# Kernel optimization log

Measured on AMD Instinct MI355X. Metric: run time of the kernel, lower is better.

Reference implementation:

```python
import jax, jax.numpy as jnp
import numpy as np

K, D, N = 32, 128, 65536
EPS = 1e-6


def setup_inputs() -> dict:
    key = jax.random.key(0)
    k1, k2, k3 = jax.random.split(key, 3)
    x = jax.random.normal(k1, (N, D), dtype=jnp.float32)
    means = jax.random.normal(k2, (K, D), dtype=jnp.float32)
    # SPD covariances (original init is identity; use SPD perturbation so Cholesky is valid)
    B = jax.random.normal(k3, (K, D, D), dtype=jnp.float32) * 0.1
    covariances = jnp.einsum('kij,klj->kil', B, B) / D + jnp.eye(D, dtype=jnp.float32)
    weights = jnp.ones((K,), dtype=jnp.float32) / K
    return {"x": x, "means": means, "covariances": covariances, "weights": weights}


def reference(x, means, covariances, weights):
    d = x.shape[-1]
    cov = covariances + EPS * jnp.eye(d, dtype=x.dtype)          # [K,D,D]
    L = jnp.linalg.cholesky(cov)                                 # [K,D,D]
    diff = x[None, :, :] - means[:, None, :]                     # [K,N,D]
    # Mahalanobis via triangular solve: m = ||L^{-1}(x-mu)||^2
    sol = jax.scipy.linalg.solve_triangular(
        L, jnp.swapaxes(diff, 1, 2), lower=True)                 # [K,D,N]
    maha = jnp.sum(sol * sol, axis=1)                            # [K,N]
    half_logdet = jnp.sum(jnp.log(jnp.diagonal(L, axis1=1, axis2=2)), axis=1)  # [K]
    log_prob = (-0.5 * (d * jnp.log(2.0 * jnp.pi) + maha)
                - half_logdet[:, None])                          # [K,N]
    weighted = log_prob.T + jnp.log(weights)                     # [N,K]
    return jax.nn.logsumexp(weighted, axis=1)                    # [N]
```

## Files before the change

### kernel.cpp

```cpp
#include <hip/hip_runtime.h>
#include <hip/hip_bf16.h>
#include <math.h>

#define KCOMP 32
#define DDIM  128
#define NPTS  65536
#define GMM_EPS 1e-6f
#define SA 129
#define UFT 1280

typedef __attribute__((ext_vector_type(8)))  __bf16 bf16x8;
typedef __attribute__((ext_vector_type(16))) float  f32x16;

__device__ __forceinline__ unsigned short f2bf(float f){
  unsigned u = __builtin_bit_cast(unsigned, f);
  u = (u + 0x7FFFu + ((u >> 16) & 1u)) >> 16;
  return (unsigned short)u;
}
__device__ __forceinline__ float rlane(float v, int lsrc){
  return __builtin_bit_cast(float, __builtin_amdgcn_readlane(__builtin_bit_cast(int, v), lsrc));
}

__device__ __noinline__ float chol_inv32(float* __restrict__ Ab,
                                         float* __restrict__ Wb,
                                         const int c){
  float ar[32], lr[32], rd[32], v[32];
  #pragma unroll
  for(int i=0;i<32;i++) ar[i] = Ab[i*SA + c];
  float hl = 0.f;
  #pragma unroll
  for(int j=0;j<32;j++){
    float d   = rlane(ar[j], j);
    float rsd = rsqrtf(d);
    hl += logf(d);
    rd[j] = rsd;
    float Lcj  = ar[j]*rsd;
    lr[j] = (c>=j) ? Lcj : 0.f;
    float coef = Lcj*rsd;
    #pragma unroll
    for(int i=j;i<32;i++){
      float bij = rlane(ar[i], j);
      ar[i] = fmaf(-bij, coef, ar[i]);
    }
  }
  #pragma unroll
  for(int j=0;j<32;j++) Ab[c*SA + j] = lr[j];
  #pragma unroll
  for(int i=0;i<32;i++){
    float s = (i==c) ? 1.f : 0.f;
    #pragma unroll
    for(int p=0;p<i;p++) s = fmaf(-rlane(lr[p], i), v[p], s);
    v[i] = s * rd[i];
  }
  #pragma unroll
  for(int i=0;i<32;i++) Wb[i*SA + c] = v[i];
  return 0.5f*hl;
}

__global__ __launch_bounds__(256) void k_prep(const float* __restrict__ cov,
                                              const float* __restrict__ wts,
                                              const float* __restrict__ means,
                                              float* __restrict__ ws_c3,
                                              unsigned short* __restrict__ qfrag,
                                              unsigned short* __restrict__ ufrag){
  __shared__ float A[DDIM*SA];
  __shared__ float W[DDIM*SA];
  __shared__ float Tb[3*32*33];
  __shared__ float muS[DDIM];
  const int t=threadIdx.x, w=t>>6, l=t&63, k=blockIdx.x;
  const int r0=(l>>3)*4, c0=(l&7)*4;

  const float4* cv4 = (const float4*)(cov + (size_t)k*DDIM*DDIM);
  #pragma unroll
  for(int v=0; v<16; v++){
    int idx4 = t + 256*v; float4 f = cv4[idx4];
    int e = idx4*4; int i = e>>7; int j = e&127;
    float* d = &A[i*SA+j]; d[0]=f.x; d[1]=f.y; d[2]=f.z; d[3]=f.w;
  }
  for(int z=t; z<DDIM*SA; z+=256) W[z] = 0.f;
  if(t<DDIM) muS[t] = means[k*DDIM+t];
  __syncthreads();
  if(t<DDIM) A[t*SA+t] += GMM_EPS;
  __syncthreads();

  static const int SYI[10]={1,2,2,3,3,3, 2,3,3, 3};
  static const int SYJ[10]={1,1,2,1,2,3, 2,2,3, 3};
  static const int SYO[5] ={0,6,9,10,10};

  float hsum = 0.f;
  #pragma unroll 1
  for(int b=0;b<4;b++){
    const int b32=b*32;
    if(w==0) hsum += chol_inv32(&A[b32*SA+b32], &W[b32*SA+b32], l&31);
    __syncthreads();
    if(w < 3-b){
      const int ibl = b+1+w;
      float acc[4][4]={};
      for(int kc=0;kc<32;kc+=4){
        float a_[4][4], b_[4][4];
        #pragma unroll
        for(int e=0;e<4;e++)
          #pragma unroll
          for(int g=0;g<4;g++){
            a_[e][g]=A[(32*ibl+r0+e)*SA + b32+kc+g];
            b_[e][g]=W[(b32+c0+e)*SA   + b32+kc+g];
          }
        #pragma unroll
        for(int e=0;e<4;e++)
          #pragma unroll
          for(int f=0;f<4;f++)
            acc[e][f]+=a_[e][0]*b_[f][0]+a_[e][1]*b_[f][1]
                      +a_[e][2]*b_[f][2]+a_[e][3]*b_[f][3];
      }
      #pragma unroll
      for(int e=0;e<4;e++)
        #pragma unroll
        for(int f=0;f<4;f++)
          A[(32*ibl+r0+e)*SA + b32+c0+f] = acc[e][f];
    }
    __syncthreads();
    #pragma unroll 1
    for(int u=SYO[b]+w; u<SYO[b+1]; u+=4){
      const int ui=SYI[u], uj=SYJ[u];
      float acc[4][4]={};
      for(int kc=0;kc<32;kc+=4){
        float a_[4][4], b_[4][4];
        #pragma unroll
        for(int e=0;e<4;e++)
          #pragma unroll
          for(int g=0;g<4;g++){
            a_[e][g]=A[(32*ui+r0+e)*SA + b32+kc+g];
            b_[e][g]=A[(32*uj+c0+e)*SA + b32+kc+g];
          }
        #pragma unroll
        for(int e=0;e<4;e++)
          #pragma unroll
          for(int f=0;f<4;f++)
            acc[e][f]+=a_[e][0]*b_[f][0]+a_[e][1]*b_[f][1]
                      +a_[e][2]*b_[f][2]+a_[e][3]*b_[f][3];
      }
      #pragma unroll
      for(int e=0;e<4;e++)
        #pragma unroll
        for(int f=0;f<4;f++)
          A[(32*ui+r0+e)*SA+32*uj+c0+f] -= acc[e][f];
    }
    __syncthreads();
  }

  #pragma unroll 1
  for(int lev=1;lev<=3;lev++){
    if(w<4-lev){
      const int j=w, i=w+lev;
      float* T=&Tb[w*1056];
      float acc[4][4]={};
      #pragma unroll 1
      for(int p=j;p<i;p++){
        for(int kc=0;kc<32;kc+=4){
          float a_[4][4], b_[4][4];
          #pragma unroll
          for(int e=0;e<4;e++)
            #pragma unroll
            for(int g=0;g<4;g++){
              a_[e][g]=A[(32*i+r0+e)*SA + 32*p+kc+g];
              b_[e][g]=W[(32*p+kc+e)*SA + 32*j+c0+g];
            }
          #pragma unroll
          for(int e=0;e<4;e++)
            #pragma unroll
            for(int f=0;f<4;f++)
              acc[e][f]+=a_[e][0]*b_[0][f]+a_[e][1]*b_[1][f]
                        +a_[e][2]*b_[2][f]+a_[e][3]*b_[3][f];
        }
      }
      #pragma unroll
      for(int e=0;e<4;e++)
        #pragma unroll
        for(int f=0;f<4;f++)
          T[(r0+e)*33+c0+f]=acc[e][f];
      float ac2[4][4]={};
      for(int kc=0;kc<32;kc+=4){
        float a_[4][4], b_[4][4];
        #pragma unroll
        for(int e=0;e<4;e++)
          #pragma unroll
          for(int g=0;g<4;g++){
            a_[e][g]=W[(32*i+r0+e)*SA + 32*i+kc+g];
            b_[e][g]=T[(kc+e)*33 + c0+g];
          }
        #pragma unroll
        for(int e=0;e<4;e++)
          #pragma unroll
          for(int f=0;f<4;f++)
            ac2[e][f]+=a_[e][0]*b_[0][f]+a_[e][1]*b_[1][f]
                      +a_[e][2]*b_[2][f]+a_[e][3]*b_[3][f];
      }
      #pragma unroll
      for(int e=0;e<4;e++)
        #pragma unroll
        for(int f=0;f<4;f++)
          W[(32*i+r0+e)*SA+32*j+c0+f] = -ac2[e][f];
    }
    __syncthreads();
  }

  if(t<DDIM){
    float s=0.f;
    #pragma unroll 8
    for(int c=0;c<DDIM;c++) s += W[t*SA+c]*muS[c];
    Tb[t]=s;
  }
  __syncthreads();
  if(t<DDIM){
    float s=0.f;
    #pragma unroll 8
    for(int r=0;r<DDIM;r++) s += W[r*SA+t]*Tb[r];
    Tb[128+t]=s;
  }
  __syncthreads();
  if(w==0){
    float p = Tb[l]*Tb[l] + Tb[l+64]*Tb[l+64];
    #pragma unroll
    for(int off=32; off; off>>=1) p += __shfl_xor(p, off);
    if(l==0) ws_c3[k] = logf(wts[k]) - hsum - 117.6241322f - 0.5f*p;
  }
  if(t<16){
    int tile=t>>1, half=t&1;
    const float* qq=&Tb[128 + tile*16 + half*8];
    unsigned uu[4];
    #pragma unroll
    for(int h2=0;h2<4;h2++){
      unsigned lo=f2bf(qq[2*h2]), hi=f2bf(qq[2*h2+1]);
      uu[h2]=lo|(hi<<16);
    }
    uint4 wv; wv.x=uu[0]; wv.y=uu[1]; wv.z=uu[2]; wv.w=uu[3];
    ((uint4*)qfrag)[tile*64 + half*32 + k] = wv;
  }
  #pragma unroll 1
  for(int s0=t;s0<UFT;s0+=256){
    int tile=s0>>6, l2=s0&63;
    int db = (tile<2)?0:((tile<6)?1:((tile<12)?2:3));
    int kc = tile - ((db==0)?0:((db==1)?2:((db==2)?6:12)));
    int row=db*32+(l2&31), colb=kc*16+((l2>>5)<<3);
    unsigned uu[4];
    #pragma unroll
    for(int h2=0;h2<4;h2++){
      unsigned lo=f2bf(W[row*SA+colb+2*h2]);
      unsigned hi=f2bf(W[row*SA+colb+2*h2+1]);
      uu[h2]=lo|(hi<<16);
    }
    uint4 wv; wv.x=uu[0]; wv.y=uu[1]; wv.z=uu[2]; wv.w=uu[3];
    ((uint4*)ufrag)[(size_t)k*UFT+s0]=wv;
  }
}

#define MFMA_B(acc,u,xv) acc=__builtin_amdgcn_mfma_f32_32x32x16_bf16(__builtin_bit_cast(bf16x8,u),xv,acc,0,0,0)

__global__ __launch_bounds__(512,2) void k_main(const float* __restrict__ x,
                                                const uint4* __restrict__ uf,
                                                const uint4* __restrict__ qf,
                                                const float* __restrict__ ws_c3,
                                                float* __restrict__ out){
  __shared__ uint4 xs[4*8*64];
  __shared__ float lin[KCOMP*128];
  __shared__ float mahaS[4*8*128];
  __shared__ float c3s[KCOMP];
  const int t=threadIdx.x, lane=t&63, w=t>>6;
  const int qh=lane>>5, ln=lane&31;
  const size_t n0=(size_t)blockIdx.x*128;

  if(t<KCOMP) c3s[t]=ws_c3[t];

  {
    const float* xb = x + n0*DDIM;
    #pragma unroll
    for(int j=0;j<8;j++){
      int idx = j*512 + t;
      int n = idx & 127, d0 = (idx>>7)*4;
      float4 f = *(const float4*)(xb + (size_t)n*DDIM + d0);
      unsigned lo = f2bf(f.x) | (((unsigned)f2bf(f.y))<<16);
      unsigned hi = f2bf(f.z) | (((unsigned)f2bf(f.w))<<16);
      int tile=n>>5, lnn=n&31, c=d0>>4, qq=(d0>>3)&1, e4=d0&7;
      *(uint2*)((char*)xs + tile*8192 + c*1024 + qq*512 + lnn*16 + e4*2)
          = make_uint2(lo,hi);
    }
  }
  __syncthreads();

  if(w<4){
    f32x16 aq={};
    #pragma unroll
    for(int c=0;c<8;c++){
      uint4 qr = qf[c*64+lane];
      bf16x8 xq = __builtin_bit_cast(bf16x8, xs[w*512 + c*64 + lane]);
      MFMA_B(aq, qr, xq);
    }
    #pragma unroll
    for(int r=0;r<16;r++){
      int row=(r&3)+8*(r>>2)+4*qh;
      lin[row*128 + w*32 + ln] = -2.f*aq[r];
    }
  }

  #pragma unroll 1
  for(int iter=0;iter<4;iter++){
    const int k = iter*8 + w;
    uint4 ur[20];
    #pragma unroll
    for(int j=0;j<20;j++) ur[j]=uf[(size_t)k*UFT + j*64 + lane];

    #pragma unroll 1
    for(int tile=0;tile<4;tile++){
      bf16x8 xf[8];
      #pragma unroll
      for(int c=0;c<8;c++) xf[c]=__builtin_bit_cast(bf16x8, xs[tile*512 + c*64 + lane]);
      f32x16 a0={},a1={},a2={},a3={};
      #pragma unroll
      for(int c=0;c<2;c++) MFMA_B(a0, ur[c],    xf[c]);
      #pragma unroll
      for(int c=0;c<4;c++) MFMA_B(a1, ur[2+c],  xf[c]);
      #pragma unroll
      for(int c=0;c<6;c++) MFMA_B(a2, ur[6+c],  xf[c]);
      #pragma unroll
      for(int c=0;c<8;c++) MFMA_B(a3, ur[12+c], xf[c]);
      float p0=0.f,p1=0.f,p2=0.f,p3=0.f;
      #pragma unroll
      for(int r=0;r<16;r+=2){
        p0=fmaf(a0[r],a0[r],p0); p1=fmaf(a0[r+1],a0[r+1],p1);
        p2=fmaf(a1[r],a1[r],p2); p3=fmaf(a1[r+1],a1[r+1],p3);
        p0=fmaf(a2[r],a2[r],p0); p1=fmaf(a2[r+1],a2[r+1],p1);
        p2=fmaf(a3[r],a3[r],p2); p3=fmaf(a3[r+1],a3[r+1],p3);
      }
      float p=(p0+p1)+(p2+p3);
      p += __shfl_xor(p,32);
      if(qh==0) mahaS[iter*1024 + w*128 + tile*32 + ln] = p;
    }
  }
  __syncthreads();

  if(t<128){
    float m_run=-INFINITY, s_run=0.f;
    #pragma unroll 1
    for(int k3=0;k3<KCOMP;k3++){
      float a  = c3s[k3] - 0.5f*(mahaS[(k3>>3)*1024 + (k3&7)*128 + t] + lin[k3*128 + t]);
      float nm = fmaxf(m_run,a);
      s_run = s_run*__expf(m_run-nm)+__expf(a-nm);
      m_run = nm;
    }
    out[n0+t] = m_run + logf(s_run);
  }
}

extern "C" void kernel_launch(void* const* d_in, const int* in_sizes, int n_in,
                              void* d_out, int out_size, void* d_ws, size_t ws_size,
                              hipStream_t stream){
  const float* x   = (const float*)d_in[0];
  const float* mu  = (const float*)d_in[1];
  const float* cov = (const float*)d_in[2];
  const float* wts = (const float*)d_in[3];
  float* out = (float*)d_out;
  char*  ws  = (char*)d_ws;

  float*          wsC3 = (float*)ws;
  unsigned short* wsQF = (unsigned short*)(ws + 512);
  unsigned short* wsUF = (unsigned short*)(ws + 16384);

  k_prep<<<KCOMP, 256, 0, stream>>>(cov, wts, mu, wsC3, wsQF, wsUF);
  k_main<<<NPTS/128, 512, 0, stream>>>(x, (const uint4*)wsUF, (const uint4*)wsQF, wsC3, out);
}
```

Before: 193.5 us.

## Reschedule blocked Cholesky and inverse into hand-overlapped wave stages

The per-component prep kernel's blocked Cholesky, triangular inversion and fragment packing are rewritten as an explicit stage schedule. Each wave runs a different panel, syrk, inverse or pack unit in the same barrier interval, so the serial diagonal factorization overlaps with other work and fewer barriers leave waves idle. The diagonal block routine now computes the log-determinant from one log of its own diagonal entry instead of 32 logs per lane, and uses a column-oriented forward substitution. The hand-written schedule is easy to get wrong in its dependencies, and the win is limited to the prep kernel, which is probably a small part of total time next to the main kernel.

```diff
diff --git a/kernel.cpp b/kernel.cpp
--- a/kernel.cpp
+++ b/kernel.cpp
@@ -24,21 +24,21 @@
 __device__ __noinline__ float chol_inv32(float* __restrict__ Ab,
                                          float* __restrict__ Wb,
                                          const int c){
-  float ar[32], lr[32], rd[32], v[32];
+  float ar[32], lr[32], rd[32], s[32];
   #pragma unroll
   for(int i=0;i<32;i++) ar[i] = Ab[i*SA + c];
-  float hl = 0.f;
+  float mydiag = 1.f;
   #pragma unroll
   for(int j=0;j<32;j++){
     float d   = rlane(ar[j], j);
     float rsd = rsqrtf(d);
-    hl += logf(d);
     rd[j] = rsd;
     float Lcj  = ar[j]*rsd;
     lr[j] = (c>=j) ? Lcj : 0.f;
+    if(c==j) mydiag = Lcj;
     float coef = Lcj*rsd;
     #pragma unroll
-    for(int i=j;i<32;i++){
+    for(int i=j+1;i<32;i++){
       float bij = rlane(ar[i], j);
       ar[i] = fmaf(-bij, coef, ar[i]);
     }
@@ -46,15 +46,143 @@
   #pragma unroll
   for(int j=0;j<32;j++) Ab[c*SA + j] = lr[j];
   #pragma unroll
-  for(int i=0;i<32;i++){
-    float s = (i==c) ? 1.f : 0.f;
-    #pragma unroll
-    for(int p=0;p<i;p++) s = fmaf(-rlane(lr[p], i), v[p], s);
-    v[i] = s * rd[i];
-  }
-  #pragma unroll
-  for(int i=0;i<32;i++) Wb[i*SA + c] = v[i];
-  return 0.5f*hl;
+  for(int i=0;i<32;i++) s[i] = (i==c) ? 1.f : 0.f;
+  #pragma unroll
+  for(int j=0;j<32;j++){
+    float vj = s[j]*rd[j];
+    s[j] = vj;
+    #pragma unroll
+    for(int i=j+1;i<32;i++)
+      s[i] = fmaf(-rlane(lr[j], i), vj, s[i]);
+  }
+  #pragma unroll
+  for(int i=0;i<32;i++) Wb[i*SA + c] = s[i];
+  return logf(mydiag);
+}
+
+__device__ __forceinline__ void panel_unit(float* __restrict__ A, const float* __restrict__ W,
+                                           int r0, int c0, int b, int ibl){
+  const int b32=b*32;
+  float acc[4][4]={};
+  for(int kc=0;kc<32;kc+=4){
+    float a_[4][4], b_[4][4];
+    #pragma unroll
+    for(int e=0;e<4;e++)
+      #pragma unroll
+      for(int g=0;g<4;g++){
+        a_[e][g]=A[(32*ibl+r0+e)*SA + b32+kc+g];
+        b_[e][g]=W[(b32+c0+e)*SA   + b32+kc+g];
+      }
+    #pragma unroll
+    for(int e=0;e<4;e++)
+      #pragma unroll
+      for(int f=0;f<4;f++)
+        acc[e][f]+=a_[e][0]*b_[f][0]+a_[e][1]*b_[f][1]
+                  +a_[e][2]*b_[f][2]+a_[e][3]*b_[f][3];
+  }
+  #pragma unroll
+  for(int e=0;e<4;e++)
+    #pragma unroll
+    for(int f=0;f<4;f++)
+      A[(32*ibl+r0+e)*SA + b32+c0+f] = acc[e][f];
+}
+
+__device__ __forceinline__ void syrk_unit(float* __restrict__ A,
+                                          int r0, int c0, int b, int ui, int uj){
+  const int b32=b*32;
+  float acc[4][4]={};
+  for(int kc=0;kc<32;kc+=4){
+    float a_[4][4], b_[4][4];
+    #pragma unroll
+    for(int e=0;e<4;e++)
+      #pragma unroll
+      for(int g=0;g<4;g++){
+        a_[e][g]=A[(32*ui+r0+e)*SA + b32+kc+g];
+        b_[e][g]=A[(32*uj+c0+e)*SA + b32+kc+g];
+      }
+    #pragma unroll
+    for(int e=0;e<4;e++)
+      #pragma unroll
+      for(int f=0;f<4;f++)
+        acc[e][f]+=a_[e][0]*b_[f][0]+a_[e][1]*b_[f][1]
+                  +a_[e][2]*b_[f][2]+a_[e][3]*b_[f][3];
+  }
+  #pragma unroll
+  for(int e=0;e<4;e++)
+    #pragma unroll
+    for(int f=0;f<4;f++)
+      A[(32*ui+r0+e)*SA+32*uj+c0+f] -= acc[e][f];
+}
+
+__device__ __forceinline__ void tg_unit(const float* __restrict__ A, const float* __restrict__ W,
+                                        float* __restrict__ T, int r0, int c0, int i, int j){
+  float acc[4][4]={};
+  #pragma unroll 1
+  for(int p=j;p<i;p++){
+    for(int kc=0;kc<32;kc+=4){
+      float a_[4][4], b_[4][4];
+      #pragma unroll
+      for(int e=0;e<4;e++)
+        #pragma unroll
+        for(int g=0;g<4;g++){
+          a_[e][g]=A[(32*i+r0+e)*SA + 32*p+kc+g];
+          b_[e][g]=W[(32*p+kc+e)*SA + 32*j+c0+g];
+        }
+      #pragma unroll
+      for(int e=0;e<4;e++)
+        #pragma unroll
+        for(int f=0;f<4;f++)
+          acc[e][f]+=a_[e][0]*b_[0][f]+a_[e][1]*b_[1][f]
+                    +a_[e][2]*b_[2][f]+a_[e][3]*b_[3][f];
+    }
+  }
+  #pragma unroll
+  for(int e=0;e<4;e++)
+    #pragma unroll
+    for(int f=0;f<4;f++)
+      T[(r0+e)*33+c0+f]=acc[e][f];
+}
+
+__device__ __forceinline__ void a2_unit(float* __restrict__ W, const float* __restrict__ T,
+                                        int r0, int c0, int i, int j){
+  float ac2[4][4]={};
+  for(int kc=0;kc<32;kc+=4){
+    float a_[4][4], b_[4][4];
+    #pragma unroll
+    for(int e=0;e<4;e++)
+      #pragma unroll
+      for(int g=0;g<4;g++){
+        a_[e][g]=W[(32*i+r0+e)*SA + 32*i+kc+g];
+        b_[e][g]=T[(kc+e)*33 + c0+g];
+      }
+    #pragma unroll
+    for(int e=0;e<4;e++)
+      #pragma unroll
+      for(int f=0;f<4;f++)
+        ac2[e][f]+=a_[e][0]*b_[0][f]+a_[e][1]*b_[1][f]
+                  +a_[e][2]*b_[2][f]+a_[e][3]*b_[3][f];
+  }
+  #pragma unroll
+  for(int e=0;e<4;e++)
+    #pragma unroll
+    for(int f=0;f<4;f++)
+      W[(32*i+r0+e)*SA+32*j+c0+f] = -ac2[e][f];
+}
+
+__device__ __forceinline__ void pack_tile(const float* __restrict__ W,
+                                          uint4* __restrict__ uf4, int tile, int l){
+  int db = (tile<2)?0:((tile<6)?1:((tile<12)?2:3));
+  int kc = tile - ((db==0)?0:((db==1)?2:((db==2)?6:12)));
+  int row=db*32+(l&31), colb=kc*16+((l>>5)<<3);
+  unsigned uu[4];
+  #pragma unroll
+  for(int h2=0;h2<4;h2++){
+    unsigned lo=f2bf(W[row*SA+colb+2*h2]);
+    unsigned hi=f2bf(W[row*SA+colb+2*h2+1]);
+    uu[h2]=lo|(hi<<16);
+  }
+  uint4 wv; wv.x=uu[0]; wv.y=uu[1]; wv.z=uu[2]; wv.w=uu[3];
+  uf4[tile*64 + l] = wv;
 }
 
 __global__ __launch_bounds__(256) void k_prep(const float* __restrict__ cov,
@@ -65,10 +193,12 @@
                                               unsigned short* __restrict__ ufrag){
   __shared__ float A[DDIM*SA];
   __shared__ float W[DDIM*SA];
-  __shared__ float Tb[3*32*33];
+  __shared__ float Tb[3*1056];
   __shared__ float muS[DDIM];
+  __shared__ float mq[256];
   const int t=threadIdx.x, w=t>>6, l=t&63, k=blockIdx.x;
   const int r0=(l>>3)*4, c0=(l&7)*4;
+  uint4* ufK = (uint4*)ufrag + (size_t)k*UFT;
 
   const float4* cv4 = (const float4*)(cov + (size_t)k*DDIM*DDIM);
   #pragma unroll
@@ -83,150 +213,92 @@
   if(t<DDIM) A[t*SA+t] += GMM_EPS;
   __syncthreads();
 
-  static const int SYI[10]={1,2,2,3,3,3, 2,3,3, 3};
-  static const int SYJ[10]={1,1,2,1,2,3, 2,2,3, 3};
-  static const int SYO[5] ={0,6,9,10,10};
-
-  float hsum = 0.f;
-  #pragma unroll 1
-  for(int b=0;b<4;b++){
-    const int b32=b*32;
-    if(w==0) hsum += chol_inv32(&A[b32*SA+b32], &W[b32*SA+b32], l&31);
-    __syncthreads();
-    if(w < 3-b){
-      const int ibl = b+1+w;
-      float acc[4][4]={};
-      for(int kc=0;kc<32;kc+=4){
-        float a_[4][4], b_[4][4];
-        #pragma unroll
-        for(int e=0;e<4;e++)
-          #pragma unroll
-          for(int g=0;g<4;g++){
-            a_[e][g]=A[(32*ibl+r0+e)*SA + b32+kc+g];
-            b_[e][g]=W[(b32+c0+e)*SA   + b32+kc+g];
-          }
-        #pragma unroll
-        for(int e=0;e<4;e++)
-          #pragma unroll
-          for(int f=0;f<4;f++)
-            acc[e][f]+=a_[e][0]*b_[f][0]+a_[e][1]*b_[f][1]
-                      +a_[e][2]*b_[f][2]+a_[e][3]*b_[f][3];
-      }
-      #pragma unroll
-      for(int e=0;e<4;e++)
-        #pragma unroll
-        for(int f=0;f<4;f++)
-          A[(32*ibl+r0+e)*SA + b32+c0+f] = acc[e][f];
-    }
-    __syncthreads();
-    #pragma unroll 1
-    for(int u=SYO[b]+w; u<SYO[b+1]; u+=4){
-      const int ui=SYI[u], uj=SYJ[u];
-      float acc[4][4]={};
-      for(int kc=0;kc<32;kc+=4){
-        float a_[4][4], b_[4][4];
-        #pragma unroll
-        for(int e=0;e<4;e++)
-          #pragma unroll
-          for(int g=0;g<4;g++){
-            a_[e][g]=A[(32*ui+r0+e)*SA + b32+kc+g];
-            b_[e][g]=A[(32*uj+c0+e)*SA + b32+kc+g];
-          }
-        #pragma unroll
-        for(int e=0;e<4;e++)
-          #pragma unroll
-          for(int f=0;f<4;f++)
-            acc[e][f]+=a_[e][0]*b_[f][0]+a_[e][1]*b_[f][1]
-                      +a_[e][2]*b_[f][2]+a_[e][3]*b_[f][3];
-      }
-      #pragma unroll
-      for(int e=0;e<4;e++)
-        #pragma unroll
-        for(int f=0;f<4;f++)
-          A[(32*ui+r0+e)*SA+32*uj+c0+f] -= acc[e][f];
-    }
-    __syncthreads();
-  }
-
-  #pragma unroll 1
-  for(int lev=1;lev<=3;lev++){
-    if(w<4-lev){
-      const int j=w, i=w+lev;
-      float* T=&Tb[w*1056];
-      float acc[4][4]={};
-      #pragma unroll 1
-      for(int p=j;p<i;p++){
-        for(int kc=0;kc<32;kc+=4){
-          float a_[4][4], b_[4][4];
-          #pragma unroll
-          for(int e=0;e<4;e++)
-            #pragma unroll
-            for(int g=0;g<4;g++){
-              a_[e][g]=A[(32*i+r0+e)*SA + 32*p+kc+g];
-              b_[e][g]=W[(32*p+kc+e)*SA + 32*j+c0+g];
-            }
-          #pragma unroll
-          for(int e=0;e<4;e++)
-            #pragma unroll
-            for(int f=0;f<4;f++)
-              acc[e][f]+=a_[e][0]*b_[0][f]+a_[e][1]*b_[1][f]
-                        +a_[e][2]*b_[2][f]+a_[e][3]*b_[3][f];
-        }
-      }
-      #pragma unroll
-      for(int e=0;e<4;e++)
-        #pragma unroll
-        for(int f=0;f<4;f++)
-          T[(r0+e)*33+c0+f]=acc[e][f];
-      float ac2[4][4]={};
-      for(int kc=0;kc<32;kc+=4){
-        float a_[4][4], b_[4][4];
-        #pragma unroll
-        for(int e=0;e<4;e++)
-          #pragma unroll
-          for(int g=0;g<4;g++){
-            a_[e][g]=W[(32*i+r0+e)*SA + 32*i+kc+g];
-            b_[e][g]=T[(kc+e)*33 + c0+g];
-          }
-        #pragma unroll
-        for(int e=0;e<4;e++)
-          #pragma unroll
-          for(int f=0;f<4;f++)
-            ac2[e][f]+=a_[e][0]*b_[0][f]+a_[e][1]*b_[1][f]
-                      +a_[e][2]*b_[2][f]+a_[e][3]*b_[3][f];
-      }
-      #pragma unroll
-      for(int e=0;e<4;e++)
-        #pragma unroll
-        for(int f=0;f<4;f++)
-          W[(32*i+r0+e)*SA+32*j+c0+f] = -ac2[e][f];
-    }
-    __syncthreads();
-  }
-
-  if(t<DDIM){
+  float hl = 0.f;
+  if(w==0) hl += chol_inv32(&A[0], &W[0], l&31);
+  __syncthreads();
+  if(w==1)      panel_unit(A,W,r0,c0,0,1);
+  else if(w==2) panel_unit(A,W,r0,c0,0,2);
+  else if(w==3) panel_unit(A,W,r0,c0,0,3);
+  __syncthreads();
+  if(w==0)      syrk_unit(A,r0,c0,0,1,1);
+  else if(w==1) syrk_unit(A,r0,c0,0,2,1);
+  else if(w==2) syrk_unit(A,r0,c0,0,3,1);
+  else          syrk_unit(A,r0,c0,0,2,2);
+  __syncthreads();
+  if(w==0)      hl += chol_inv32(&A[32*SA+32], &W[32*SA+32], l&31);
+  else if(w==1) syrk_unit(A,r0,c0,0,3,2);
+  else if(w==2) syrk_unit(A,r0,c0,0,3,3);
+  __syncthreads();
+  if(w==1)      panel_unit(A,W,r0,c0,1,2);
+  else if(w==2) panel_unit(A,W,r0,c0,1,3);
+  else if(w==3) tg_unit(A,W,&Tb[0],r0,c0,1,0);
+  __syncthreads();
+  if(w==0)      syrk_unit(A,r0,c0,1,2,2);
+  else if(w==1) a2_unit(W,&Tb[0],r0,c0,1,0);
+  else if(w==2) tg_unit(A,W,&Tb[1056],r0,c0,2,1);
+  else          syrk_unit(A,r0,c0,1,3,2);
+  __syncthreads();
+  if(w==0)      hl += chol_inv32(&A[64*SA+64], &W[64*SA+64], l&31);
+  else if(w==1) syrk_unit(A,r0,c0,1,3,3);
+  else if(w==2) tg_unit(A,W,&Tb[0],r0,c0,2,0);
+  __syncthreads();
+  if(w==1)      panel_unit(A,W,r0,c0,2,3);
+  else if(w==2) a2_unit(W,&Tb[0],r0,c0,2,0);
+  else if(w==3) a2_unit(W,&Tb[1056],r0,c0,2,1);
+  __syncthreads();
+  if(w==0)      syrk_unit(A,r0,c0,2,3,3);
+  else if(w==1) tg_unit(A,W,&Tb[0],r0,c0,3,0);
+  else if(w==2) tg_unit(A,W,&Tb[1056],r0,c0,3,1);
+  else          tg_unit(A,W,&Tb[2112],r0,c0,3,2);
+  __syncthreads();
+  if(w==0)      hl += chol_inv32(&A[96*SA+96], &W[96*SA+96], l&31);
+  else if(w==1 || (w==2 && l<32)){
+    int r = (w==1)? l : 64+l;
     float s=0.f;
     #pragma unroll 8
-    for(int c=0;c<DDIM;c++) s += W[t*SA+c]*muS[c];
-    Tb[t]=s;
-  }
-  __syncthreads();
-  if(t<DDIM){
+    for(int c=0;c<DDIM;c++) s += W[r*SA+c]*muS[c];
+    mq[r]=s;
+  }
+  __syncthreads();
+  if(w==1)      a2_unit(W,&Tb[0],r0,c0,3,0);
+  else if(w==2) a2_unit(W,&Tb[1056],r0,c0,3,1);
+  else if(w==3) a2_unit(W,&Tb[2112],r0,c0,3,2);
+  __syncthreads();
+  if(w==0){
+    if(l<32){
+      int r = 96+l;
+      float s=0.f;
+      #pragma unroll 8
+      for(int c=0;c<DDIM;c++) s += W[r*SA+c]*muS[c];
+      mq[r]=s;
+    }
+  } else {
+    #pragma unroll
+    for(int j=0;j<4;j++) pack_tile(W, ufK, (w-1)*4+j, l);
+  }
+  __syncthreads();
+  if(t<128){
     float s=0.f;
     #pragma unroll 8
-    for(int r=0;r<DDIM;r++) s += W[r*SA+t]*Tb[r];
-    Tb[128+t]=s;
+    for(int r=0;r<DDIM;r++) s += W[r*SA+t]*mq[r];
+    mq[128+t]=s;
+  } else if(w==2){
+    #pragma unroll
+    for(int j=0;j<4;j++) pack_tile(W, ufK, 12+j, l);
+  } else {
+    #pragma unroll
+    for(int j=0;j<4;j++) pack_tile(W, ufK, 16+j, l);
   }
   __syncthreads();
   if(w==0){
-    float p = Tb[l]*Tb[l] + Tb[l+64]*Tb[l+64];
-    #pragma unroll
-    for(int off=32; off; off>>=1) p += __shfl_xor(p, off);
-    if(l==0) ws_c3[k] = logf(wts[k]) - hsum - 117.6241322f - 0.5f*p;
-  }
-  if(t<16){
-    int tile=t>>1, half=t&1;
-    const float* qq=&Tb[128 + tile*16 + half*8];
+    float hv = (l<32)? hl : 0.f;
+    float p  = mq[l]*mq[l] + mq[l+64]*mq[l+64];
+    #pragma unroll
+    for(int off=32; off; off>>=1){ hv += __shfl_xor(hv,off); p += __shfl_xor(p,off); }
+    if(l==0) ws_c3[k] = logf(wts[k]) - hv - 117.6241322f - 0.5f*p;
+  } else if(w==1 && l<16){
+    int tile=l>>1, half=l&1;
+    const float* qq=&mq[128 + tile*16 + half*8];
     unsigned uu[4];
     #pragma unroll
     for(int h2=0;h2<4;h2++){
@@ -235,22 +307,6 @@
     }
     uint4 wv; wv.x=uu[0]; wv.y=uu[1]; wv.z=uu[2]; wv.w=uu[3];
     ((uint4*)qfrag)[tile*64 + half*32 + k] = wv;
-  }
-  #pragma unroll 1
-  for(int s0=t;s0<UFT;s0+=256){
-    int tile=s0>>6, l2=s0&63;
-    int db = (tile<2)?0:((tile<6)?1:((tile<12)?2:3));
-    int kc = tile - ((db==0)?0:((db==1)?2:((db==2)?6:12)));
-    int row=db*32+(l2&31), colb=kc*16+((l2>>5)<<3);
-    unsigned uu[4];
-    #pragma unroll
-    for(int h2=0;h2<4;h2++){
-      unsigned lo=f2bf(W[row*SA+colb+2*h2]);
-      unsigned hi=f2bf(W[row*SA+colb+2*h2+1]);
-      uu[h2]=lo|(hi<<16);
-    }
-    uint4 wv; wv.x=uu[0]; wv.y=uu[1]; wv.z=uu[2]; wv.w=uu[3];
-    ((uint4*)ufrag)[(size_t)k*UFT+s0]=wv;
   }
 }
 
```

Result: faster. 171.7 us, median of 2 (-11.3%).
